# Performance work log

Hardware: AMD Instinct MI355X
Metric: run time of the kernel (lower is better)

Reference implementation:

```python
import jax, jax.numpy as jnp
import numpy as np

N_EMBD = 1024
N_HEAD = 16
HEAD_DIM = N_EMBD // N_HEAD  # 64
LATENT_DIM = N_EMBD // 2     # 512
B, T = 4, 2048


def setup_inputs() -> dict:
    key = jax.random.key(0)
    ks = jax.random.split(key, 5)
    # weights stored [in, out] so forward is x @ W (equivalent to torch Linear with W.T)
    def init(k, fan_in, fan_out):
        bound = 1.0 / np.sqrt(fan_in)
        return jax.random.uniform(k, (fan_in, fan_out), jnp.float32, -bound, bound)
    return {
        "x": jax.random.normal(ks[0], (B, T, N_EMBD), jnp.float32),
        "Wc_down": init(ks[1], N_EMBD, LATENT_DIM),
        "Wq_up": init(ks[2], LATENT_DIM, N_EMBD),
        "Wkv_up": init(ks[3], LATENT_DIM, 2 * HEAD_DIM),
        "Wc_proj": init(ks[4], N_EMBD, N_EMBD),
    }


def reference(x, Wc_down, Wq_up, Wkv_up, Wc_proj):
    Bsz, Tlen, C = x.shape
    latent = x @ Wc_down                                    # [B,T,latent]
    q = (latent @ Wq_up).reshape(Bsz, Tlen, N_HEAD, HEAD_DIM)  # [B,T,H,D]
    kv = latent @ Wkv_up                                    # [B,T,2D]
    k, v = kv[..., :HEAD_DIM], kv[..., HEAD_DIM:]           # shared across heads (MQA)
    scale = 1.0 / np.sqrt(HEAD_DIM)
    att = jnp.einsum("bthd,bsd->bhts", q, k) * scale        # [B,H,T,T]
    causal = jnp.tril(jnp.ones((Tlen, Tlen), dtype=bool))
    att = jnp.where(causal[None, None], att, -jnp.inf)
    att = jax.nn.softmax(att, axis=-1)
    y = jnp.einsum("bhts,bsd->bthd", att, v).reshape(Bsz, Tlen, C)
    return y @ Wc_proj
```

## Files before the change

kernel.cpp:

```cpp
#include <hip/hip_runtime.h>
#include <hip/hip_bf16.h>


typedef __attribute__((ext_vector_type(8))) short bf16x8;
typedef __attribute__((ext_vector_type(4))) float floatx4;
typedef __attribute__((ext_vector_type(4))) unsigned int uintx4;

#define B_   4
#define T_   2048
#define C_   1024
#define H_   16
#define D_   64
#define L_   512
#define QKV_N 1152

__device__ __forceinline__ float EXP2F(float x) {
    float r;
    asm("v_exp_f32 %0, %1" : "=v"(r) : "v"(x));
    return r;
}

__device__ __forceinline__ unsigned short f2bf(float f) {
    unsigned int x = __float_as_uint(f);
    unsigned int r = (x + 0x7fffu + ((x >> 16) & 1u)) >> 16;
    return (unsigned short)r;
}

__device__ __forceinline__ unsigned int cvtpk_bf(float lo, float hi) {
    unsigned int r;
    asm("v_cvt_pk_bf16_f32 %0, %1, %2" : "=v"(r) : "v"(lo), "v"(hi));
    return r;
}

__device__ __forceinline__ void pl32(unsigned int& d, unsigned int& s) {
    asm("v_permlane32_swap_b32 %0, %1" : "+v"(d), "+v"(s));
}
__device__ __forceinline__ void pl16(unsigned int& d, unsigned int& s) {
    asm("v_permlane16_swap_b32 %0, %1" : "+v"(d), "+v"(s));
}

__device__ __forceinline__ void gload_lds16(const unsigned short* g, char* l) {
    __builtin_amdgcn_global_load_lds(
        (const __attribute__((address_space(1))) void*)g,
        (__attribute__((address_space(3))) void*)l,
        16, 0, 0);
}

__global__ __launch_bounds__(256) void prep(const float* __restrict__ x, unsigned short* __restrict__ xb,
                                            const float* __restrict__ Wd, unsigned short* __restrict__ wdb,
                                            const float* __restrict__ Wq, const float* __restrict__ Wkv,
                                            unsigned short* __restrict__ wqkvT,
                                            const float* __restrict__ Wp, unsigned short* __restrict__ wpT,
                                            float ksc) {
    const int bid = blockIdx.x;
    const int tid = threadIdx.x;
    if (bid < 8192) {
        int i = bid * 256 + tid;
        float4 v = *(const float4*)(x + (size_t)i * 4);
        ushort4 o;
        o.x = f2bf(v.x); o.y = f2bf(v.y); o.z = f2bf(v.z); o.w = f2bf(v.w);
        *(ushort4*)(xb + (size_t)i * 4) = o;
    } else if (bid < 8704) {
        int i = (bid - 8192) * 256 + tid;
        float4 v = *(const float4*)(Wd + (size_t)i * 4);
        ushort4 o;
        o.x = f2bf(v.x); o.y = f2bf(v.y); o.z = f2bf(v.z); o.w = f2bf(v.w);
        *(ushort4*)(wdb + (size_t)i * 4) = o;
    } else if (bid < 10752) {
        int idx = (bid - 8704) * 256 + tid;
        int n = idx >> 9, k = idx & 511;
        wqkvT[idx] = f2bf(Wq[(size_t)k * 1024 + n] * ksc);
    } else if (bid < 11008) {
        int idx = (bid - 10752) * 256 + tid;
        int n = idx >> 9, k = idx & 511;
        wqkvT[1024 * 512 + idx] = f2bf(Wkv[(size_t)k * 128 + n]);
    } else {
        int idx = (bid - 11008) * 256 + tid;
        int n = idx >> 10, k = idx & 1023;
        wpT[idx] = f2bf(Wp[(size_t)k * 1024 + n]);
    }
}

#define BM 128
#define BN 128
#define BK 64

template <bool F32OUT, bool VTFOLD>
__global__ __launch_bounds__(256) void gemm_bt(const unsigned short* __restrict__ A,
                                               const unsigned short* __restrict__ Bt,
                                               void* __restrict__ Cout,
                                               unsigned short* __restrict__ Vtf,
                                               int M, int N, int K, int nbx) {
    __shared__ __align__(16) char ldsA[2][BM * BK * 2];
    __shared__ __align__(16) char ldsB[2][BN * BK * 2];
    const int tid = threadIdx.x;
    const int lane = tid & 63, wave = tid >> 6;
    const int lrow = lane & 15, lhi = lane >> 4;

    const int bid = blockIdx.x;
    const int cpx = gridDim.x >> 3;
    const int swz = (bid & 7) * cpx + (bid >> 3);
    const int by = swz / nbx, bx = swz - by * nbx;
    const int bm = by * BM, bn = bx * BN;
    const int wm = (wave >> 1) * 64, wn = (wave & 1) * 64;

    const unsigned short* ap[4];
    const unsigned short* bp[4];
#pragma unroll
    for (int i = 0; i < 4; ++i) {
        int c = tid + i * 256;
        int row = c >> 3;
        int sc = ((c & 7) ^ (row & 7)) * 8;
        ap[i] = A + (size_t)(bm + row) * K + sc;
        bp[i] = Bt + (size_t)(bn + row) * K + sc;
    }
    const int nk = K >> 6;
    floatx4 acc[4][4] = {};

#pragma unroll
    for (int i = 0; i < 4; ++i) {
        gload_lds16(ap[i], ldsA[0] + (i * 256 + wave * 64) * 16);
        gload_lds16(bp[i], ldsB[0] + (i * 256 + wave * 64) * 16);
        ap[i] += BK; bp[i] += BK;
    }

    for (int t = 0; t < nk; ++t) {
        const int cur = t & 1;
        if (t + 1 < nk) {
#pragma unroll
            for (int i = 0; i < 4; ++i) {
                gload_lds16(ap[i], ldsA[cur ^ 1] + (i * 256 + wave * 64) * 16);
                gload_lds16(bp[i], ldsB[cur ^ 1] + (i * 256 + wave * 64) * 16);
                ap[i] += BK; bp[i] += BK;
            }
            asm volatile("s_waitcnt vmcnt(8)" ::: "memory");
        } else {
            asm volatile("s_waitcnt vmcnt(0)" ::: "memory");
        }
        __builtin_amdgcn_s_barrier();
        __builtin_amdgcn_sched_barrier(0);

#pragma unroll
        for (int kk = 0; kk < 2; ++kk) {
            bf16x8 af[4], bfr[4];
#pragma unroll
            for (int m = 0; m < 4; ++m) {
                int row = wm + m * 16 + lrow;
                int colb = kk * 64 + lhi * 16;
                af[m] = *(const bf16x8*)(ldsA[cur] + row * 128 + (colb ^ ((row & 7) << 4)));
            }
#pragma unroll
            for (int n = 0; n < 4; ++n) {
                int row = wn + n * 16 + lrow;
                int colb = kk * 64 + lhi * 16;
                bfr[n] = *(const bf16x8*)(ldsB[cur] + row * 128 + (colb ^ ((row & 7) << 4)));
            }
#pragma unroll
            for (int m = 0; m < 4; ++m)
#pragma unroll
                for (int n = 0; n < 4; ++n)
                    acc[m][n] = __builtin_amdgcn_mfma_f32_16x16x32_bf16(af[m], bfr[n], acc[m][n], 0, 0, 0);
        }
        __builtin_amdgcn_sched_barrier(0);
        __builtin_amdgcn_s_barrier();
    }
#pragma unroll
    for (int m = 0; m < 4; ++m)
#pragma unroll
        for (int n = 0; n < 4; ++n)
#pragma unroll
            for (int r = 0; r < 4; ++r) {
                int row = bm + wm + m * 16 + lhi * 4 + r;
                int col = bn + wn + n * 16 + lrow;
                float v = acc[m][n][r];
                if (F32OUT)
                    ((float*)Cout)[(size_t)row * N + col] = v;
                else {
                    unsigned short bv = f2bf(v);
                    ((unsigned short*)Cout)[(size_t)row * N + col] = bv;
                    if (VTFOLD && col >= 1088) {
                        Vtf[(((size_t)(row >> 11) * 64 + (col - 1088)) << 11) | (row & 2047)] = bv;
                    }
                }
            }
}

__global__ __launch_bounds__(256, 3) void flash(const unsigned short* __restrict__ QKV,
                                                const unsigned short* __restrict__ Vt,
                                                unsigned short* __restrict__ Y) {
    const int id = blockIdx.x;
    const int qt = 15 - (id >> 6);
    const int h = (id >> 2) & 15;
    const int b = id & 3;
    const int tid = threadIdx.x;
    const int lane = tid & 63, wave = tid >> 6;
    const int lrow = lane & 15, lhi = lane >> 4;

    __shared__ __align__(16) char ldsK[3][64 * 128];
    __shared__ __align__(16) char ldsV[3][64 * 128];

    const int qbase = qt * 128 + wave * 32;
    const unsigned short* KV = QKV + 1024;
    const int nst = qt * 2 + 2;

    const unsigned short* kp[2];
    const unsigned short* vp[2];
#pragma unroll
    for (int i = 0; i < 2; ++i) {
        int c = tid + i * 256;
        int row = c >> 3;
        int sc = ((c & 7) ^ (row & 7)) * 8;
        kp[i] = KV + ((size_t)(b * T_ + row)) * QKV_N + sc;
        vp[i] = Vt + ((size_t)(b * 64 + row)) * T_ + sc;
    }

    bf16x8 qf[2][2];
#pragma unroll
    for (int nf = 0; nf < 2; ++nf)
#pragma unroll
        for (int kk = 0; kk < 2; ++kk) {
            int trow = b * T_ + qbase + nf * 16 + lrow;
            int col = h * 64 + kk * 32 + lhi * 8;
            qf[nf][kk] = *(const bf16x8*)(QKV + (size_t)trow * QKV_N + col);
        }

    floatx4 o[2][4] = {};
    floatx4 ol[2] = {};

    const short one_bf = (short)0x3F80;
    const bf16x8 ones8 = {one_bf, one_bf, one_bf, one_bf, one_bf, one_bf, one_bf, one_bf};

    char* kcur = ldsK[0];  char* kstg = ldsK[1];  char* kfre = ldsK[2];
    char* vcur = ldsV[0];  char* vstg = ldsV[1];  char* vfre = ldsV[2];
#pragma unroll
    for (int i = 0; i < 2; ++i) {
        gload_lds16(kp[i], kcur + (i * 256 + wave * 64) * 16);
        gload_lds16(vp[i], vcur + (i * 256 + wave * 64) * 16);
        kp[i] += 64 * QKV_N;
        vp[i] += 64;
    }

    for (int st = 0; st < nst; ++st) {
        const bool more = (st + 1 < nst);
        const long kadj = more ? 0 : -(long)(64 * QKV_N);
        const long vadj = more ? 0 : -64L;
#pragma unroll
        for (int i = 0; i < 2; ++i) {
            gload_lds16(kp[i] + kadj, kstg + (i * 256 + wave * 64) * 16);
            gload_lds16(vp[i] + vadj, vstg + (i * 256 + wave * 64) * 16);
        }
        if (more) {
            kp[0] += 64 * QKV_N; kp[1] += 64 * QKV_N;
            vp[0] += 64;         vp[1] += 64;
        }
        asm volatile("s_waitcnt vmcnt(4)" ::: "memory");
        __builtin_amdgcn_s_barrier();
        __builtin_amdgcn_sched_barrier(0);

        if (st * 64 <= qbase + 31) {
            floatx4 s[4][2] = {};
#pragma unroll
            for (int kk = 0; kk < 2; ++kk) {
                bf16x8 kf[4];
#pragma unroll
                for (int mf = 0; mf < 4; ++mf) {
                    int row = mf * 16 + lrow;
                    int colb = kk * 64 + lhi * 16;
                    kf[mf] = *(const bf16x8*)(kcur + row * 128 + (colb ^ ((row & 7) << 4)));
                }
                __builtin_amdgcn_s_setprio(1);
#pragma unroll
                for (int mf = 0; mf < 4; ++mf)
#pragma unroll
                    for (int nf = 0; nf < 2; ++nf)
                        s[mf][nf] = __builtin_amdgcn_mfma_f32_16x16x32_bf16(kf[mf], qf[nf][kk], s[mf][nf], 0, 0, 0);
                __builtin_amdgcn_s_setprio(0);
            }

#pragma unroll
            for (int nf = 0; nf < 2; ++nf) {
                if (st * 64 + 63 > qbase + nf * 16) {
                    int qg = qbase + nf * 16 + lrow;
#pragma unroll
                    for (int mf = 0; mf < 4; ++mf)
#pragma unroll
                        for (int r = 0; r < 4; ++r) {
                            int sg = st * 64 + mf * 16 + lhi * 4 + r;
                            if (sg > qg) s[mf][nf][r] = -1e30f;
                        }
                }
#pragma unroll
                for (int mf = 0; mf < 4; ++mf)
#pragma unroll
                    for (int rr = 0; rr < 4; ++rr)
                        s[mf][nf][rr] = EXP2F(s[mf][nf][rr]);
            }

            bf16x8 pfr[2][2];
#pragma unroll
            for (int nf = 0; nf < 2; ++nf)
#pragma unroll
                for (int ss = 0; ss < 2; ++ss) {
                    unsigned int A0 = cvtpk_bf(s[2 * ss][nf][0], s[2 * ss][nf][1]);
                    unsigned int A1 = cvtpk_bf(s[2 * ss][nf][2], s[2 * ss][nf][3]);
                    unsigned int B0 = cvtpk_bf(s[2 * ss + 1][nf][0], s[2 * ss + 1][nf][1]);
                    unsigned int B1 = cvtpk_bf(s[2 * ss + 1][nf][2], s[2 * ss + 1][nf][3]);
                    pl32(A0, B0); pl16(A0, B0);
                    pl32(A1, B1); pl16(A1, B1);
                    uintx4 pw; pw.x = A0; pw.y = A1; pw.z = B0; pw.w = B1;
                    pfr[nf][ss] = __builtin_bit_cast(bf16x8, pw);
                }

#pragma unroll
            for (int ss = 0; ss < 2; ++ss) {
                bf16x8 vf[4];
#pragma unroll
                for (int dn = 0; dn < 4; ++dn) {
                    int row = dn * 16 + lrow;
                    int colb = ss * 64 + lhi * 16;
                    vf[dn] = *(const bf16x8*)(vcur + row * 128 + (colb ^ ((row & 7) << 4)));
                }
                __builtin_amdgcn_s_setprio(1);
#pragma unroll
                for (int m = 0; m < 2; ++m) {
#pragma unroll
                    for (int dn = 0; dn < 4; ++dn)
                        o[m][dn] = __builtin_amdgcn_mfma_f32_16x16x32_bf16(pfr[m][ss], vf[dn], o[m][dn], 0, 0, 0);
                    ol[m] = __builtin_amdgcn_mfma_f32_16x16x32_bf16(pfr[m][ss], ones8, ol[m], 0, 0, 0);
                }
                __builtin_amdgcn_s_setprio(0);
            }
        }

        char* t;
        t = kcur; kcur = kstg; kstg = kfre; kfre = t;
        t = vcur; vcur = vstg; vstg = vfre; vfre = t;
    }

#pragma unroll
    for (int m = 0; m < 2; ++m) {
        float linv[4];
#pragma unroll
        for (int rr = 0; rr < 4; ++rr) linv[rr] = __builtin_amdgcn_rcpf(ol[m][rr]);
#pragma unroll
        for (int dn = 0; dn < 4; ++dn)
#pragma unroll
            for (int rr = 0; rr < 4; ++rr) {
                int trow = b * T_ + qbase + m * 16 + lhi * 4 + rr;
                int col = h * 64 + dn * 16 + lrow;
                Y[(size_t)trow * C_ + col] = f2bf(o[m][dn][rr] * linv[rr]);
            }
    }
}

extern "C" void kernel_launch(void* const* d_in, const int* in_sizes, int n_in,
                              void* d_out, int out_size, void* d_ws, size_t ws_size,
                              hipStream_t stream) {
    (void)in_sizes; (void)n_in; (void)out_size; (void)ws_size;
    const float* x   = (const float*)d_in[0];
    const float* Wd  = (const float*)d_in[1];
    const float* Wq  = (const float*)d_in[2];
    const float* Wkv = (const float*)d_in[3];
    const float* Wp  = (const float*)d_in[4];
    float* out = (float*)d_out;
    char* ws = (char*)d_ws;

    const int BT = B_ * T_;
    const float KSC = 0.125f * 1.44269504f;

    unsigned short* xb     = (unsigned short*)(ws + 0);
    unsigned short* wqkvT  = (unsigned short*)(ws + 16777216);
    unsigned short* wdb    = (unsigned short*)(ws + 17956864);
    unsigned short* wpT    = (unsigned short*)(ws + 19005440);
    unsigned short* wcombT = (unsigned short*)(ws + 21102592);
    unsigned short* qkv    = (unsigned short*)(ws + 29491200);
    unsigned short* vt     = (unsigned short*)(ws + 48365568);
    unsigned short* yb     = xb;

    prep<<<15104, 256, 0, stream>>>(x, xb, Wd, wdb, Wq, Wkv, wqkvT, Wp, wpT, KSC);

    gemm_bt<false, false><<<8 * 9, 256, 0, stream>>>(wqkvT, wdb, wcombT, nullptr, QKV_N, C_, L_, 8);

    gemm_bt<false, true><<<9 * 64, 256, 0, stream>>>(xb, wcombT, qkv, vt, BT, QKV_N, C_, 9);

    flash<<<1024, 256, 0, stream>>>(qkv, vt, yb);

    gemm_bt<true, false><<<8 * 64, 256, 0, stream>>>(yb, wpT, out, nullptr, BT, C_, C_, 8);
}
```

Before: 135.6 us.

## Split flash attention KV range in two halves and merge with combine kernel

Each query tile's causal KV range is split into two equal halves handled by separate blocks, doubling the flash grid. Each block writes unnormalized bf16 partial outputs and per-row sums. A new combine kernel adds the partials and divides by the summed denominators. This aims to improve CU occupancy and load balance across the causal triangle, at the cost of an extra elementwise kernel, extra memory traffic, bf16 rounding of partial sums, and reuse of the output buffer as scratch.

New measurement: 142.0 us. 1.05x slower.

```diff
diff --git a/kernel.cpp b/kernel.cpp
--- a/kernel.cpp
+++ b/kernel.cpp
@@ -45,6 +45,9 @@
         (__attribute__((address_space(3))) void*)l,
         16, 0, 0);
 }
+
+__device__ __forceinline__ float lo16f(unsigned int w) { return __uint_as_float(w << 16); }
+__device__ __forceinline__ float hi16f(unsigned int w) { return __uint_as_float(w & 0xffff0000u); }
 
 __global__ __launch_bounds__(256) void prep(const float* __restrict__ x, unsigned short* __restrict__ xb,
                                             const float* __restrict__ Wd, unsigned short* __restrict__ wdb,
@@ -187,11 +190,15 @@
 
 __global__ __launch_bounds__(256, 3) void flash(const unsigned short* __restrict__ QKV,
                                                 const unsigned short* __restrict__ Vt,
-                                                unsigned short* __restrict__ Y) {
+                                                unsigned short* __restrict__ N0,
+                                                unsigned short* __restrict__ N1,
+                                                float* __restrict__ Lh) {
     const int id = blockIdx.x;
-    const int qt = 15 - (id >> 6);
-    const int h = (id >> 2) & 15;
-    const int b = id & 3;
+    const int qt = 15 - (id >> 7);
+    const int r7 = id & 127;
+    const int half = r7 >> 6;
+    const int h = (r7 >> 2) & 15;
+    const int b = r7 & 3;
     const int tid = threadIdx.x;
     const int lane = tid & 63, wave = tid >> 6;
     const int lrow = lane & 15, lhi = lane >> 4;
@@ -201,7 +208,8 @@
 
     const int qbase = qt * 128 + wave * 32;
     const unsigned short* KV = QKV + 1024;
-    const int nst = qt * 2 + 2;
+    const int s0 = half * (qt + 1);
+    const int s1 = s0 + (qt + 1);
 
     const unsigned short* kp[2];
     const unsigned short* vp[2];
@@ -210,8 +218,8 @@
         int c = tid + i * 256;
         int row = c >> 3;
         int sc = ((c & 7) ^ (row & 7)) * 8;
-        kp[i] = KV + ((size_t)(b * T_ + row)) * QKV_N + sc;
-        vp[i] = Vt + ((size_t)(b * 64 + row)) * T_ + sc;
+        kp[i] = KV + ((size_t)(b * T_ + s0 * 64 + row)) * QKV_N + sc;
+        vp[i] = Vt + ((size_t)(b * 64 + row)) * T_ + s0 * 64 + sc;
     }
 
     bf16x8 qf[2][2];
@@ -240,8 +248,8 @@
         vp[i] += 64;
     }
 
-    for (int st = 0; st < nst; ++st) {
-        const bool more = (st + 1 < nst);
+    for (int st = s0; st < s1; ++st) {
+        const bool more = (st + 1 < s1);
         const long kadj = more ? 0 : -(long)(64 * QKV_N);
         const long vadj = more ? 0 : -64L;
 #pragma unroll
@@ -337,20 +345,51 @@
         t = vcur; vcur = vstg; vstg = vfre; vfre = t;
     }
 
-#pragma unroll
-    for (int m = 0; m < 2; ++m) {
-        float linv[4];
-#pragma unroll
-        for (int rr = 0; rr < 4; ++rr) linv[rr] = __builtin_amdgcn_rcpf(ol[m][rr]);
+    unsigned short* Nout = half ? N1 : N0;
+#pragma unroll
+    for (int m = 0; m < 2; ++m)
 #pragma unroll
         for (int dn = 0; dn < 4; ++dn)
 #pragma unroll
             for (int rr = 0; rr < 4; ++rr) {
                 int trow = b * T_ + qbase + m * 16 + lhi * 4 + rr;
                 int col = h * 64 + dn * 16 + lrow;
-                Y[(size_t)trow * C_ + col] = f2bf(o[m][dn][rr] * linv[rr]);
-            }
-    }
+                Nout[(size_t)trow * C_ + col] = f2bf(o[m][dn][rr]);
+            }
+    if (lrow == 0) {
+#pragma unroll
+        for (int m = 0; m < 2; ++m)
+#pragma unroll
+            for (int rr = 0; rr < 4; ++rr) {
+                int qrow = qbase + m * 16 + lhi * 4 + rr;
+                Lh[half * (4 * 2048 * 16) + ((b * 2048 + qrow) << 4) + h] = ol[m][rr];
+            }
+    }
+}
+
+__global__ __launch_bounds__(256) void combine(unsigned short* __restrict__ N0,
+                                               const unsigned short* __restrict__ N1,
+                                               const float* __restrict__ Lh) {
+    const int i = blockIdx.x * 256 + threadIdx.x;
+    const int row = i >> 7;
+    const int c0 = (i & 127) * 8;
+    const int b = row >> 11, t = row & 2047;
+    const int h = c0 >> 6;
+    const float l = Lh[((b * 2048 + t) << 4) + h] + Lh[4 * 2048 * 16 + ((b * 2048 + t) << 4) + h];
+    const float linv = __builtin_amdgcn_rcpf(l);
+
+    uintx4 a = *(const uintx4*)(N0 + (size_t)row * C_ + c0);
+    uintx4 c = *(const uintx4*)(N1 + (size_t)row * C_ + c0);
+    uintx4 out;
+#pragma unroll
+    for (int j = 0; j < 4; ++j) {
+        unsigned int aw = ((const unsigned int*)&a)[j];
+        unsigned int cw = ((const unsigned int*)&c)[j];
+        float ylo = (lo16f(aw) + lo16f(cw)) * linv;
+        float yhi = (hi16f(aw) + hi16f(cw)) * linv;
+        ((unsigned int*)&out)[j] = cvtpk_bf(ylo, yhi);
+    }
+    *(uintx4*)(N0 + (size_t)row * C_ + c0) = out;
 }
 
 extern "C" void kernel_launch(void* const* d_in, const int* in_sizes, int n_in,
@@ -369,12 +408,14 @@
     const float KSC = 0.125f * 1.44269504f;
 
     unsigned short* xb     = (unsigned short*)(ws + 0);
-    unsigned short* wqkvT  = (unsigned short*)(ws + 16777216);
-    unsigned short* wdb    = (unsigned short*)(ws + 17956864);
-    unsigned short* wpT    = (unsigned short*)(ws + 19005440);
-    unsigned short* wcombT = (unsigned short*)(ws + 21102592);
-    unsigned short* qkv    = (unsigned short*)(ws + 29491200);
-    unsigned short* vt     = (unsigned short*)(ws + 48365568);
+    unsigned short* qkv    = (unsigned short*)(ws + 16777216);
+    unsigned short* vt     = (unsigned short*)(ws + 35651584);
+    unsigned short* wpT    = (unsigned short*)(ws + 36700160);
+    unsigned short* wqkvT  = (unsigned short*)(ws + 38797312);
+    unsigned short* wdb    = (unsigned short*)(ws + 39976960);
+    unsigned short* wcombT = (unsigned short*)(ws + 41025536);
+    float*          lh     = (float*)(ws + 43384832);
+    unsigned short* n1     = (unsigned short*)d_out;
     unsigned short* yb     = xb;
 
     prep<<<15104, 256, 0, stream>>>(x, xb, Wd, wdb, Wq, Wkv, wqkvT, Wp, wpT, KSC);
@@ -383,7 +424,9 @@
 
     gemm_bt<false, true><<<9 * 64, 256, 0, stream>>>(xb, wcombT, qkv, vt, BT, QKV_N, C_, 9);
 
-    flash<<<1024, 256, 0, stream>>>(qkv, vt, yb);
+    flash<<<2048, 256, 0, stream>>>(qkv, vt, xb, n1, lh);
+
+    combine<<<4096, 256, 0, stream>>>(xb, n1, lh);
 
     gemm_bt<true, false><<<8 * 64, 256, 0, stream>>>(yb, wpT, out, nullptr, BT, C_, C_, 8);
 }
```
